# Performance work log

Measured on AMD Instinct MI355X. Metric: run time of the kernel, lower is better.

Reference implementation:

```python
import jax, jax.numpy as jnp
import numpy as np

# ---- static config ----
G = 4          # num graphs
NG = 512       # nodes per graph
N = G * NG     # total nodes
E = 32768      # num edges
IN_DIM = 128
HID = 32
HEADS = 4
HC = HID * HEADS  # 128
OUT_DIM = 32
N_LAYERS = 2
GRID = 500
Q = 20
NEG_SLOPE = 0.2
QUANTILES = jnp.asarray(np.linspace(0.0, 1.0, Q), jnp.float32)  # [Q]


def setup_inputs() -> dict:
    key = jax.random.key(0)
    ks = jax.random.split(key, 32)
    inp = {}
    inp['x'] = jax.random.normal(ks[0], (N, IN_DIM), jnp.float32)
    inp['edge_index'] = jax.random.randint(ks[1], (2, E), 0, N).astype(jnp.int64)
    inp['batch'] = (jnp.arange(N) // NG).astype(jnp.int64)
    # GATConv params (2 layers, both 128 -> 4 heads x 32, concat)
    for l, (kin,) in enumerate([(IN_DIM,), (HC,)]):
        s = 1.0 / np.sqrt(kin)
        inp[f'W{l}'] = jax.random.normal(ks[2 + 4 * l], (kin, HC), jnp.float32) * s
        inp[f'as{l}'] = jax.random.normal(ks[3 + 4 * l], (HEADS, HID), jnp.float32) * s
        inp[f'ad{l}'] = jax.random.normal(ks[4 + 4 * l], (HEADS, HID), jnp.float32) * s
        inp[f'b{l}'] = jnp.zeros((HC,), jnp.float32)
    for l in range(N_LAYERS + 1):
        inp[f'lpW{l}'] = jax.random.normal(ks[10 + 2 * l], (HC, OUT_DIM), jnp.float32) * (1.0 / np.sqrt(HC))
        inp[f'lpb{l}'] = jnp.zeros((OUT_DIM,), jnp.float32)
    for l in range(N_LAYERS + 1):
        inp[f'kW{l}'] = jax.random.normal(ks[16 + 2 * l], (HC * Q, OUT_DIM), jnp.float32) * (1.0 / np.sqrt(HC * Q))
        inp[f'kb{l}'] = jnp.zeros((OUT_DIM,), jnp.float32)
    inp['pool_w'] = jnp.ones((2,), jnp.float32) / 2.0
    inp['beta'] = jax.random.normal(ks[22], (OUT_DIM,), jnp.float32)
    inp['h0'] = jax.random.normal(ks[23], (1,), jnp.float32)
    return inp


def _gat_layer(x, src, dst, W, a_src, a_dst, bias):
    # PyG GATConv (concat=True, add_self_loops=True, negative_slope=0.2), eval mode
    n = x.shape[0]
    xh = (x @ W).reshape(n, HEADS, HID)              # [N,H,C]
    loop = jnp.arange(n)
    s = jnp.concatenate([src, loop])                 # [E+N]
    d = jnp.concatenate([dst, loop])
    al_s = jnp.einsum('nhc,hc->nh', xh, a_src)       # [N,H]
    al_d = jnp.einsum('nhc,hc->nh', xh, a_dst)
    e = jax.nn.leaky_relu(al_s[s] + al_d[d], NEG_SLOPE)   # [E+N,H]
    e_max = jax.ops.segment_max(e, d, num_segments=n)     # stable softmax per dst
    e = jnp.exp(e - e_max[d])
    denom = jax.ops.segment_sum(e, d, num_segments=n)
    alpha = e / (denom[d] + 1e-16)                   # [E+N,H]
    out = jax.ops.segment_sum(alpha[:, :, None] * xh[s], d, num_segments=n)
    return out.reshape(n, HC) + bias


def _kde_per_graph(xg):
    # xg: [Ng, D] -> [D*Q] soft-quantile features via grid KDE
    n = xg.shape[0]
    mn = xg.min(axis=0) - 1e-6                       # [D]
    mx = xg.max(axis=0) + 1e-6
    grid = jnp.linspace(0.0, 1.0, GRID)[:, None] * (mx - mn) + mn   # [Gp,D]
    std = xg.std(axis=0) + 1e-8 / 3
    h = 1.06 * std * float(n) ** (-0.2)              # [D]
    u = (grid[:, None, :] - xg[None, :, :]) / h      # [Gp,Ng,D]  (dominant tensor)
    kern = jnp.exp(-0.5 * u * u) / (h * np.sqrt(2.0 * np.pi))
    density = kern.mean(axis=1)                      # [Gp,D]
    cdf = jnp.cumsum(density, axis=0)
    cdf = cdf / jnp.clip(cdf[-1:], 1e-8)
    dist = jnp.abs(cdf[:, :, None] - QUANTILES)      # [Gp,D,Q]
    w = jax.nn.sigmoid(-100.0 * dist)
    w = w / (w.sum(axis=0, keepdims=True) + 1e-8)
    qv = (grid[:, :, None] * w).sum(axis=0)          # [D,Q]
    return qv.reshape(-1)


def _readout(cur, lpW, lpb, kW, kb, pool_w):
    xr = cur.reshape(G, NG, -1)
    pooled = jnp.stack([xr.mean(axis=1), xr.max(axis=1)], axis=0)   # [2,G,D]
    wp = (pooled * pool_w[:, None, None]).sum(axis=0)               # [G,D]
    h = wp @ lpW + lpb                                              # [G,out]
    kf = jax.vmap(_kde_per_graph)(xr)                               # [G,D*Q]
    return h, kf @ kW + kb


def reference(x, edge_index, batch, W0, as0, ad0, b0, W1, as1, ad1, b1,
              lpW0, lpb0, lpW1, lpb1, lpW2, lpb2,
              kW0, kb0, kW1, kb1, kW2, kb2, pool_w, beta, h0):
    src, dst = edge_index[0], edge_index[1]
    convs = [(W0, as0, ad0, b0), (W1, as1, ad1, b1)]
    lps = [(lpW0, lpb0), (lpW1, lpb1), (lpW2, lpb2)]
    kps = [(kW0, kb0), (kW1, kb1), (kW2, kb2)]
    cur = x
    h_list, kde_list = [], []
    for i in range(N_LAYERS):
        h, kp = _readout(cur, lps[i][0], lps[i][1], kps[i][0], kps[i][1], pool_w)
        h_list.append(h); kde_list.append(kp)
        cur = _gat_layer(cur, src, dst, *convs[i])
        if i != N_LAYERS - 1:
            cur = jax.nn.relu(cur)
    h, kp = _readout(cur, lps[-1][0], lps[-1][1], kps[-1][0], kps[-1][1], pool_w)
    h_list.append(h); kde_list.append(kp)
    main_out = jnp.stack(h_list).mean(axis=0)        # [G,out]
    kde_out = jnp.stack(kde_list).mean(axis=0)
    risk = (main_out + kde_out) @ beta + h0          # [G]
    return risk
```

## Files before the change

### kernel.cpp

```cpp
#include <hip/hip_runtime.h>
#include <math.h>

#define GNUM 4
#define NG 512
#define NN 2048
#define EE 32768
#define HC 128
#define HEADS 4
#define HID 32
#define GRID_PTS 500
#define QN 20
#define ODIM 32
#define MAXE 160

#define LOG2E 1.44269504088896340736f
#define NEG_HALF_LOG2E -0.72134752044448170368f
#define N_POW_M02 0.2871745887492588f
#define SIG_K 144.269504089f

__device__ __forceinline__ float fexp2(float x){ return __builtin_amdgcn_exp2f(x); }
__device__ __forceinline__ float frcp(float x){ return __builtin_amdgcn_rcpf(x); }

__global__ __launch_bounds__(1024) void k_zero(int* __restrict__ pos, float* __restrict__ acc){
  int t = threadIdx.x;
  pos[t] = 0; pos[t+1024] = 0;
  if (t < 768) acc[t] = 0.f;
}

__global__ __launch_bounds__(512) void k_layer(const float* __restrict__ cur, int do_relu,
        const float* __restrict__ kW, const float* __restrict__ kb, float* __restrict__ kacc,
        const float* __restrict__ lpW, const float* __restrict__ lpb,
        const float* __restrict__ poolw, float* __restrict__ macc,
        const float* __restrict__ W, const float* __restrict__ as_, const float* __restrict__ ad_,
        float* __restrict__ xh, float* __restrict__ als, float* __restrict__ ald,
        int do_fill, const int* __restrict__ src, const int* __restrict__ dst,
        int* __restrict__ pos, int* __restrict__ csr_src){
  int t = threadIdx.x;
  if (blockIdx.x < 512){
    int g = blockIdx.x >> 7, d = blockIdx.x & 127;
    int lane = t & 63, wave = t >> 6;
    __shared__ __align__(16) float2 xs[NG];
    __shared__ float4 wred4[8];
    __shared__ float sc[4];
    __shared__ float wsum[8], woff[9];
    __shared__ float redw[QN][8], redg[QN][8];
    __shared__ float qs[QN];

    float v = cur[((size_t)g*NG + t)*HC + d];
    if (do_relu) v = fmaxf(v, 0.f);
    xs[t] = make_float2(v, v*v);
    float mn=v, mx=v, sm=v, sq=v*v;
    #pragma unroll
    for (int m=32; m>0; m>>=1){
      mn = fminf(mn, __shfl_xor(mn, m, 64));
      mx = fmaxf(mx, __shfl_xor(mx, m, 64));
      sm += __shfl_xor(sm, m, 64);
      sq += __shfl_xor(sq, m, 64);
    }
    if (lane==0) wred4[wave] = make_float4(mn,mx,sm,sq);
    __syncthreads();
    if (t==0){
      float4 r = wred4[0];
      #pragma unroll
      for (int i=1;i<8;++i){
        float4 b = wred4[i];
        r.x = fminf(r.x,b.x); r.y = fmaxf(r.y,b.y); r.z += b.z; r.w += b.w;
      }
      float mean = r.z * (1.f/NG);
      float var  = fmaxf(r.w*(1.f/NG) - mean*mean, 0.f);
      float sd   = sqrtf(var) + (1e-8f/3.f);
      float h    = 1.06f * sd * N_POW_M02;
      float lo = r.x - 1e-6f, hi = r.y + 1e-6f;
      sc[0] = lo;
      sc[1] = (hi-lo)*(1.f/(GRID_PTS-1));
      sc[2] = NEG_HALF_LOG2E/(h*h);
      sc[3] = poolw[0]*mean + poolw[1]*r.y;
    }
    __syncthreads();
    float lo = sc[0], st = sc[1], kk = sc[2];
    float gv = lo + st*(float)t;
    float acc = 0.f;
    if (t < GRID_PTS){
      float c0 = kk*gv*gv, c1 = -2.f*kk*gv;
      const float4* p4 = (const float4*)xs;
      #pragma unroll 4
      for (int i=0;i<NG/2;++i){
        float4 s2 = p4[i];
        acc += fexp2(fmaf(kk, s2.y, fmaf(c1, s2.x, c0)));
        acc += fexp2(fmaf(kk, s2.w, fmaf(c1, s2.z, c0)));
      }
    }
    float sv = acc;
    #pragma unroll
    for (int off=1; off<64; off<<=1){
      float n = __shfl_up(sv, off, 64);
      if (lane >= off) sv += n;
    }
    if (lane==63) wsum[wave] = sv;
    __syncthreads();
    if (t==0){
      float r2 = 0.f;
      #pragma unroll
      for (int i=0;i<8;++i){ woff[i]=r2; r2+=wsum[i]; }
      woff[8]=r2;
    }
    if (t < QN*8){ ((float*)redw)[t]=0.f; ((float*)redg)[t]=0.f; }
    __syncthreads();
    float invt = 1.f/fmaxf(woff[8], 1e-8f);
    float c = (sv + woff[wave]) * invt;
    float cw0 = __shfl(c, 0, 64), cw1 = __shfl(c, 63, 64);
    int qlo = max(0, (int)ceilf((cw0 - 0.17f)*(float)(QN-1)));
    int qhi = min(QN-1, (int)floorf((cw1 + 0.17f)*(float)(QN-1)));
    for (int q=qlo; q<=qhi; ++q){
      float w = 0.f;
      if (t < GRID_PTS){
        float dist = fabsf(c - (float)q*(1.f/(QN-1)));
        w = frcp(1.f + fexp2(SIG_K*dist));
      }
      float gw = gv*w;
      #pragma unroll
      for (int m=32;m>0;m>>=1){
        w  += __shfl_xor(w,  m, 64);
        gw += __shfl_xor(gw, m, 64);
      }
      if (lane==0){ redw[q][wave]=w; redg[q][wave]=gw; }
    }
    __syncthreads();
    if (t < QN){
      float sw=0.f, sgw=0.f;
      #pragma unroll
      for (int i=0;i<8;++i){ sw+=redw[t][i]; sgw+=redg[t][i]; }
      qs[t] = sgw / (sw + 1e-8f);
    }
    __syncthreads();
    if (t < ODIM){
      float a = 0.f;
      const float* kwb = kW + (size_t)d*QN*ODIM + t;
      #pragma unroll
      for (int q=0;q<QN;++q) a += qs[q]*kwb[q*ODIM];
      if (d==0) a += kb[t];
      atomicAdd(&kacc[g*ODIM + t], a);
      float b = sc[3]*lpW[d*ODIM + t];
      if (d==0) b += lpb[t];
      atomicAdd(&macc[g*ODIM + t], b);
    }
  } else {
    int b2 = blockIdx.x - 512;
    if (do_fill){
      int e = b2*512 + t;
      if (e < EE){
        int dd = dst[e];
        int p = atomicAdd(&pos[dd], 1);
        if (p < MAXE) csr_src[dd*MAXE + p] = src[e];
      }
    }
    int ln = t >> 7, j = t & 127;
    int n = b2*4 + ln;
    __shared__ float rows[4][HC];
    float v = cur[(size_t)n*HC + j];
    if (do_relu) v = fmaxf(v, 0.f);
    rows[ln][j] = v;
    __syncthreads();
    float acc = 0.f;
    #pragma unroll 8
    for (int c2=0;c2<HC;++c2)
      acc += rows[ln][c2]*W[(size_t)c2*HC + j];
    xh[(size_t)n*HC + j] = acc;
    int h = j >> 5, cc = j & 31;
    float ps = acc*as_[h*HID+cc], pd = acc*ad_[h*HID+cc];
    #pragma unroll
    for (int m=16;m>0;m>>=1){
      ps += __shfl_xor(ps, m, 32);
      pd += __shfl_xor(pd, m, 32);
    }
    if (cc==0){ als[n*HEADS+h]=ps; ald[n*HEADS+h]=pd; }
  }
}

__global__ __launch_bounds__(128) void k_gather(const int* __restrict__ csr_src,
        const int* __restrict__ pos,
        const float* __restrict__ als, const float* __restrict__ ald,
        const float* __restrict__ xh, const float* __restrict__ bias,
        float* __restrict__ out){
  int d = blockIdx.x, t = threadIdx.x;
  int deg = min(pos[d], MAXE-1);
  int E = deg + 1;
  const int* base = csr_src + d*MAXE;
  __shared__ int ssrc[MAXE];
  __shared__ float sexp[MAXE][HEADS];
  __shared__ float smax[HEADS], sfac[HEADS];
  float a0 = ald[d*4+0], a1 = ald[d*4+1], a2 = ald[d*4+2], a3 = ald[d*4+3];
  for (int i=t; i<E; i+=128){
    int s = (i < deg) ? base[i] : d;
    ssrc[i] = s;
    float e0 = als[s*4+0]+a0, e1 = als[s*4+1]+a1, e2 = als[s*4+2]+a2, e3 = als[s*4+3]+a3;
    e0 = (e0>=0.f)? e0 : 0.2f*e0;
    e1 = (e1>=0.f)? e1 : 0.2f*e1;
    e2 = (e2>=0.f)? e2 : 0.2f*e2;
    e3 = (e3>=0.f)? e3 : 0.2f*e3;
    sexp[i][0]=e0; sexp[i][1]=e1; sexp[i][2]=e2; sexp[i][3]=e3;
  }
  __syncthreads();
  if (t < HEADS){
    float m = -INFINITY;
    for (int i=0;i<E;++i) m = fmaxf(m, sexp[i][t]);
    smax[t] = m;
  }
  __syncthreads();
  for (int i=t; i<E; i+=128){
    #pragma unroll
    for (int h=0;h<HEADS;++h)
      sexp[i][h] = fexp2(LOG2E*(sexp[i][h]-smax[h]));
  }
  __syncthreads();
  if (t < HEADS){
    float sdn = 0.f;
    for (int i=0;i<E;++i) sdn += sexp[i][t];
    sfac[t] = 1.f/(sdn + 1e-16f);
  }
  __syncthreads();
  int h = t >> 5;
  float fac = sfac[h];
  float acc = bias[t];
  for (int i=0;i<E;++i)
    acc += sexp[i][h]*fac * xh[(size_t)ssrc[i]*HC + t];
  out[(size_t)d*HC + t] = acc;
}

__global__ void k_final(const float* __restrict__ macc, const float* __restrict__ kacc,
                        const float* __restrict__ beta, const float* __restrict__ h0,
                        float* __restrict__ out){
  int t = threadIdx.x;
  int g = t >> 5, o = t & 31;
  __shared__ float sdm[128];
  float s3 = macc[t] + macc[t+128] + macc[t+256]
           + kacc[t] + kacc[t+128] + kacc[t+256];
  sdm[t] = s3 * (1.f/3.f) * beta[o];
  __syncthreads();
  if ((t & 31) == 0){
    float s = 0.f;
    #pragma unroll
    for (int i=0;i<32;++i) s += sdm[g*32+i];
    out[g] = s + h0[0];
  }
}

extern "C" void kernel_launch(void* const* d_in, const int* in_sizes, int n_in,
                              void* d_out, int out_size, void* d_ws, size_t ws_size,
                              hipStream_t stream) {
  (void)in_sizes; (void)n_in; (void)out_size; (void)ws_size;
  const float* x    = (const float*)d_in[0];
  const int*   ei   = (const int*)d_in[1];
  const int*   srcp = ei;
  const int*   dstp = ei + EE;
  const float* W[2]   = {(const float*)d_in[3], (const float*)d_in[7]};
  const float* As[2]  = {(const float*)d_in[4], (const float*)d_in[8]};
  const float* Ad[2]  = {(const float*)d_in[5], (const float*)d_in[9]};
  const float* Bi[2]  = {(const float*)d_in[6], (const float*)d_in[10]};
  const float* lpW[3] = {(const float*)d_in[11], (const float*)d_in[13], (const float*)d_in[15]};
  const float* lpb[3] = {(const float*)d_in[12], (const float*)d_in[14], (const float*)d_in[16]};
  const float* kW[3]  = {(const float*)d_in[17], (const float*)d_in[19], (const float*)d_in[21]};
  const float* kb[3]  = {(const float*)d_in[18], (const float*)d_in[20], (const float*)d_in[22]};
  const float* poolw  = (const float*)d_in[23];
  const float* beta   = (const float*)d_in[24];
  const float* h0     = (const float*)d_in[25];
  float* out = (float*)d_out;

  float* ws = (float*)d_ws;
  float* cur1   = ws;
  float* cur2   = cur1 + 262144;
  float* xh     = cur2 + 262144;
  float* als    = xh + 262144;
  float* ald    = als + 8192;
  float* macc   = ald + 8192;
  float* kacc   = macc + 384;
  int*   pos     = (int*)(kacc + 384);
  int*   csr_src = pos + 2048;

  k_zero<<<1, 1024, 0, stream>>>(pos, macc);

  k_layer<<<1024, 512, 0, stream>>>(x, 0, kW[0], kb[0], kacc, lpW[0], lpb[0], poolw, macc,
                                    W[0], As[0], Ad[0], xh, als, ald,
                                    1, srcp, dstp, pos, csr_src);
  k_gather<<<NN, 128, 0, stream>>>(csr_src, pos, als, ald, xh, Bi[0], cur1);

  k_layer<<<1024, 512, 0, stream>>>(cur1, 1, kW[1], kb[1], kacc+128, lpW[1], lpb[1], poolw, macc+128,
                                    W[1], As[1], Ad[1], xh, als, ald,
                                    0, srcp, dstp, pos, csr_src);
  k_gather<<<NN, 128, 0, stream>>>(csr_src, pos, als, ald, xh, Bi[1], cur2);

  k_layer<<<512, 512, 0, stream>>>(cur2, 0, kW[2], kb[2], kacc+256, lpW[2], lpb[2], poolw, macc+256,
                                   nullptr, nullptr, nullptr, nullptr, nullptr, nullptr,
                                   0, nullptr, nullptr, nullptr, nullptr);

  k_final<<<1, 128, 0, stream>>>(macc, kacc, beta, h0, out);
}
```

Before: 211.0 us.

## Fuse all layers into one cooperative persistent kernel with grid syncs

Replaces the sequence of seven kernel launches with a single cooperative kernel of 512 blocks that runs the KDE readout, X·W projection, and attention gather phases back to back, separated by grid-wide syncs. Each block now does both a KDE column and four rows of the projection serially rather than in separate blocks, and the gather handles four destination nodes per 512-thread block. The aim is to remove launch and inter-kernel gaps, at the cost of serialising the KDE and XW work within a block and adding grid barriers. A fallback path with the old multi-kernel structure runs if the cooperative launch fails.

```diff
diff --git a/kernel.cpp b/kernel.cpp
--- a/kernel.cpp
+++ b/kernel.cpp
@@ -1,5 +1,7 @@
 #include <hip/hip_runtime.h>
+#include <hip/hip_cooperative_groups.h>
 #include <math.h>
+namespace cg = cooperative_groups;
 
 #define GNUM 4
 #define NG 512
@@ -12,6 +14,7 @@
 #define QN 20
 #define ODIM 32
 #define MAXE 160
+#define NBLK 512
 
 #define LOG2E 1.44269504088896340736f
 #define NEG_HALF_LOG2E -0.72134752044448170368f
@@ -21,227 +24,333 @@
 __device__ __forceinline__ float fexp2(float x){ return __builtin_amdgcn_exp2f(x); }
 __device__ __forceinline__ float frcp(float x){ return __builtin_amdgcn_rcpf(x); }
 
-__global__ __launch_bounds__(1024) void k_zero(int* __restrict__ pos, float* __restrict__ acc){
-  int t = threadIdx.x;
-  pos[t] = 0; pos[t+1024] = 0;
-  if (t < 768) acc[t] = 0.f;
-}
-
-__global__ __launch_bounds__(512) void k_layer(const float* __restrict__ cur, int do_relu,
+struct SmemKDE {
+  __align__(16) float2 xs[NG];
+  float4 wred4[8];
+  float sc[4];
+  float wsum[8], woff[9];
+  float redw[QN][8], redg[QN][8];
+  float qs[QN];
+};
+struct SmemXW  { float rows[4][HC]; };
+struct SmemGat {
+  int   ssrc[4][MAXE];
+  float sexp[4][MAXE][HEADS];
+  float smax[4][HEADS], sfac[4][HEADS];
+};
+union Smem { SmemKDE kde; SmemXW xw; SmemGat gat; };
+
+struct Params {
+  const float *x;
+  const int *src, *dst;
+  const float *W[2], *As[2], *Ad[2], *Bi[2];
+  const float *lpW[3], *lpb[3], *kW[3], *kb[3];
+  const float *poolw, *beta, *h0;
+  float *out;
+  float *cur1, *cur2, *xh, *als, *ald, *macc, *kacc;
+  int *pos, *csr;
+};
+
+__device__ void kde_phase(Smem& sm, const float* __restrict__ cur, int do_relu,
         const float* __restrict__ kW, const float* __restrict__ kb, float* __restrict__ kacc,
         const float* __restrict__ lpW, const float* __restrict__ lpb,
-        const float* __restrict__ poolw, float* __restrict__ macc,
+        const float* __restrict__ poolw, float* __restrict__ macc){
+  int b = blockIdx.x;
+  int g = b >> 7, d = b & 127;
+  int t = threadIdx.x;
+  int lane = t & 63, wave = t >> 6;
+  float v = cur[((size_t)g*NG + t)*HC + d];
+  if (do_relu) v = fmaxf(v, 0.f);
+  sm.kde.xs[t] = make_float2(v, v*v);
+  float mn=v, mx=v, smv=v, sq=v*v;
+  #pragma unroll
+  for (int m=32; m>0; m>>=1){
+    mn = fminf(mn, __shfl_xor(mn, m, 64));
+    mx = fmaxf(mx, __shfl_xor(mx, m, 64));
+    smv += __shfl_xor(smv, m, 64);
+    sq += __shfl_xor(sq, m, 64);
+  }
+  if (lane==0) sm.kde.wred4[wave] = make_float4(mn,mx,smv,sq);
+  __syncthreads();
+  if (t==0){
+    float4 r = sm.kde.wred4[0];
+    #pragma unroll
+    for (int i=1;i<8;++i){
+      float4 bb = sm.kde.wred4[i];
+      r.x = fminf(r.x,bb.x); r.y = fmaxf(r.y,bb.y); r.z += bb.z; r.w += bb.w;
+    }
+    float mean = r.z * (1.f/NG);
+    float var  = fmaxf(r.w*(1.f/NG) - mean*mean, 0.f);
+    float sd   = sqrtf(var) + (1e-8f/3.f);
+    float h    = 1.06f * sd * N_POW_M02;
+    float lo = r.x - 1e-6f, hi = r.y + 1e-6f;
+    sm.kde.sc[0] = lo;
+    sm.kde.sc[1] = (hi-lo)*(1.f/(GRID_PTS-1));
+    sm.kde.sc[2] = NEG_HALF_LOG2E/(h*h);
+    sm.kde.sc[3] = poolw[0]*mean + poolw[1]*r.y;
+  }
+  __syncthreads();
+  float lo = sm.kde.sc[0], st = sm.kde.sc[1], kk = sm.kde.sc[2];
+  float gv = lo + st*(float)t;
+  float acc = 0.f;
+  if (t < GRID_PTS){
+    float c0 = kk*gv*gv, c1 = -2.f*kk*gv;
+    const float4* p4 = (const float4*)sm.kde.xs;
+    #pragma unroll 4
+    for (int i=0;i<NG/2;++i){
+      float4 s2 = p4[i];
+      acc += fexp2(fmaf(kk, s2.y, fmaf(c1, s2.x, c0)));
+      acc += fexp2(fmaf(kk, s2.w, fmaf(c1, s2.z, c0)));
+    }
+  }
+  float sv = acc;
+  #pragma unroll
+  for (int off=1; off<64; off<<=1){
+    float n = __shfl_up(sv, off, 64);
+    if (lane >= off) sv += n;
+  }
+  if (lane==63) sm.kde.wsum[wave] = sv;
+  __syncthreads();
+  if (t==0){
+    float r2 = 0.f;
+    #pragma unroll
+    for (int i=0;i<8;++i){ sm.kde.woff[i]=r2; r2+=sm.kde.wsum[i]; }
+    sm.kde.woff[8]=r2;
+  }
+  if (t < QN*8){ ((float*)sm.kde.redw)[t]=0.f; ((float*)sm.kde.redg)[t]=0.f; }
+  __syncthreads();
+  float invt = 1.f/fmaxf(sm.kde.woff[8], 1e-8f);
+  float c = (sv + sm.kde.woff[wave]) * invt;
+  float cw0 = __shfl(c, 0, 64), cw1 = __shfl(c, 63, 64);
+  int qlo = max(0, (int)ceilf((cw0 - 0.17f)*(float)(QN-1)));
+  int qhi = min(QN-1, (int)floorf((cw1 + 0.17f)*(float)(QN-1)));
+  for (int q=qlo; q<=qhi; ++q){
+    float w = 0.f;
+    if (t < GRID_PTS){
+      float dist = fabsf(c - (float)q*(1.f/(QN-1)));
+      w = frcp(1.f + fexp2(SIG_K*dist));
+    }
+    float gw = gv*w;
+    #pragma unroll
+    for (int m=32;m>0;m>>=1){
+      w  += __shfl_xor(w,  m, 64);
+      gw += __shfl_xor(gw, m, 64);
+    }
+    if (lane==0){ sm.kde.redw[q][wave]=w; sm.kde.redg[q][wave]=gw; }
+  }
+  __syncthreads();
+  if (t < QN){
+    float sw=0.f, sgw=0.f;
+    #pragma unroll
+    for (int i=0;i<8;++i){ sw+=sm.kde.redw[t][i]; sgw+=sm.kde.redg[t][i]; }
+    sm.kde.qs[t] = sgw / (sw + 1e-8f);
+  }
+  __syncthreads();
+  if (t < ODIM){
+    float a = 0.f;
+    const float* kwb = kW + (size_t)d*QN*ODIM + t;
+    #pragma unroll
+    for (int q=0;q<QN;++q) a += sm.kde.qs[q]*kwb[q*ODIM];
+    if (d==0) a += kb[t];
+    atomicAdd(&kacc[g*ODIM + t], a);
+    float bb = sm.kde.sc[3]*lpW[d*ODIM + t];
+    if (d==0) bb += lpb[t];
+    atomicAdd(&macc[g*ODIM + t], bb);
+  }
+  __syncthreads();
+}
+
+__device__ void xw_phase(Smem& sm, const float* __restrict__ cur, int do_relu,
         const float* __restrict__ W, const float* __restrict__ as_, const float* __restrict__ ad_,
         float* __restrict__ xh, float* __restrict__ als, float* __restrict__ ald,
         int do_fill, const int* __restrict__ src, const int* __restrict__ dst,
-        int* __restrict__ pos, int* __restrict__ csr_src){
+        int* __restrict__ pos, int* __restrict__ csr){
   int t = threadIdx.x;
-  if (blockIdx.x < 512){
-    int g = blockIdx.x >> 7, d = blockIdx.x & 127;
-    int lane = t & 63, wave = t >> 6;
-    __shared__ __align__(16) float2 xs[NG];
-    __shared__ float4 wred4[8];
-    __shared__ float sc[4];
-    __shared__ float wsum[8], woff[9];
-    __shared__ float redw[QN][8], redg[QN][8];
-    __shared__ float qs[QN];
-
-    float v = cur[((size_t)g*NG + t)*HC + d];
-    if (do_relu) v = fmaxf(v, 0.f);
-    xs[t] = make_float2(v, v*v);
-    float mn=v, mx=v, sm=v, sq=v*v;
-    #pragma unroll
-    for (int m=32; m>0; m>>=1){
-      mn = fminf(mn, __shfl_xor(mn, m, 64));
-      mx = fmaxf(mx, __shfl_xor(mx, m, 64));
-      sm += __shfl_xor(sm, m, 64);
-      sq += __shfl_xor(sq, m, 64);
-    }
-    if (lane==0) wred4[wave] = make_float4(mn,mx,sm,sq);
-    __syncthreads();
-    if (t==0){
-      float4 r = wred4[0];
-      #pragma unroll
-      for (int i=1;i<8;++i){
-        float4 b = wred4[i];
-        r.x = fminf(r.x,b.x); r.y = fmaxf(r.y,b.y); r.z += b.z; r.w += b.w;
-      }
-      float mean = r.z * (1.f/NG);
-      float var  = fmaxf(r.w*(1.f/NG) - mean*mean, 0.f);
-      float sd   = sqrtf(var) + (1e-8f/3.f);
-      float h    = 1.06f * sd * N_POW_M02;
-      float lo = r.x - 1e-6f, hi = r.y + 1e-6f;
-      sc[0] = lo;
-      sc[1] = (hi-lo)*(1.f/(GRID_PTS-1));
-      sc[2] = NEG_HALF_LOG2E/(h*h);
-      sc[3] = poolw[0]*mean + poolw[1]*r.y;
-    }
-    __syncthreads();
-    float lo = sc[0], st = sc[1], kk = sc[2];
-    float gv = lo + st*(float)t;
-    float acc = 0.f;
-    if (t < GRID_PTS){
-      float c0 = kk*gv*gv, c1 = -2.f*kk*gv;
-      const float4* p4 = (const float4*)xs;
-      #pragma unroll 4
-      for (int i=0;i<NG/2;++i){
-        float4 s2 = p4[i];
-        acc += fexp2(fmaf(kk, s2.y, fmaf(c1, s2.x, c0)));
-        acc += fexp2(fmaf(kk, s2.w, fmaf(c1, s2.z, c0)));
-      }
-    }
-    float sv = acc;
-    #pragma unroll
-    for (int off=1; off<64; off<<=1){
-      float n = __shfl_up(sv, off, 64);
-      if (lane >= off) sv += n;
-    }
-    if (lane==63) wsum[wave] = sv;
-    __syncthreads();
-    if (t==0){
-      float r2 = 0.f;
-      #pragma unroll
-      for (int i=0;i<8;++i){ woff[i]=r2; r2+=wsum[i]; }
-      woff[8]=r2;
-    }
-    if (t < QN*8){ ((float*)redw)[t]=0.f; ((float*)redg)[t]=0.f; }
-    __syncthreads();
-    float invt = 1.f/fmaxf(woff[8], 1e-8f);
-    float c = (sv + woff[wave]) * invt;
-    float cw0 = __shfl(c, 0, 64), cw1 = __shfl(c, 63, 64);
-    int qlo = max(0, (int)ceilf((cw0 - 0.17f)*(float)(QN-1)));
-    int qhi = min(QN-1, (int)floorf((cw1 + 0.17f)*(float)(QN-1)));
-    for (int q=qlo; q<=qhi; ++q){
-      float w = 0.f;
-      if (t < GRID_PTS){
-        float dist = fabsf(c - (float)q*(1.f/(QN-1)));
-        w = frcp(1.f + fexp2(SIG_K*dist));
-      }
-      float gw = gv*w;
-      #pragma unroll
-      for (int m=32;m>0;m>>=1){
-        w  += __shfl_xor(w,  m, 64);
-        gw += __shfl_xor(gw, m, 64);
-      }
-      if (lane==0){ redw[q][wave]=w; redg[q][wave]=gw; }
-    }
-    __syncthreads();
-    if (t < QN){
-      float sw=0.f, sgw=0.f;
-      #pragma unroll
-      for (int i=0;i<8;++i){ sw+=redw[t][i]; sgw+=redg[t][i]; }
-      qs[t] = sgw / (sw + 1e-8f);
-    }
-    __syncthreads();
-    if (t < ODIM){
-      float a = 0.f;
-      const float* kwb = kW + (size_t)d*QN*ODIM + t;
-      #pragma unroll
-      for (int q=0;q<QN;++q) a += qs[q]*kwb[q*ODIM];
-      if (d==0) a += kb[t];
-      atomicAdd(&kacc[g*ODIM + t], a);
-      float b = sc[3]*lpW[d*ODIM + t];
-      if (d==0) b += lpb[t];
-      atomicAdd(&macc[g*ODIM + t], b);
-    }
-  } else {
-    int b2 = blockIdx.x - 512;
-    if (do_fill){
-      int e = b2*512 + t;
-      if (e < EE){
-        int dd = dst[e];
-        int p = atomicAdd(&pos[dd], 1);
-        if (p < MAXE) csr_src[dd*MAXE + p] = src[e];
-      }
-    }
-    int ln = t >> 7, j = t & 127;
-    int n = b2*4 + ln;
-    __shared__ float rows[4][HC];
-    float v = cur[(size_t)n*HC + j];
-    if (do_relu) v = fmaxf(v, 0.f);
-    rows[ln][j] = v;
-    __syncthreads();
-    float acc = 0.f;
-    #pragma unroll 8
-    for (int c2=0;c2<HC;++c2)
-      acc += rows[ln][c2]*W[(size_t)c2*HC + j];
-    xh[(size_t)n*HC + j] = acc;
-    int h = j >> 5, cc = j & 31;
-    float ps = acc*as_[h*HID+cc], pd = acc*ad_[h*HID+cc];
-    #pragma unroll
-    for (int m=16;m>0;m>>=1){
-      ps += __shfl_xor(ps, m, 32);
-      pd += __shfl_xor(pd, m, 32);
-    }
-    if (cc==0){ als[n*HEADS+h]=ps; ald[n*HEADS+h]=pd; }
-  }
-}
-
-__global__ __launch_bounds__(128) void k_gather(const int* __restrict__ csr_src,
-        const int* __restrict__ pos,
+  if (do_fill && t < 64){
+    int e = blockIdx.x*64 + t;
+    int dd = dst[e];
+    int pp = atomicAdd(&pos[dd], 1);
+    if (pp < MAXE) csr[dd*MAXE + pp] = src[e];
+  }
+  int ln = t >> 7, j = t & 127;
+  int n = blockIdx.x*4 + ln;
+  float v = cur[(size_t)n*HC + j];
+  if (do_relu) v = fmaxf(v, 0.f);
+  sm.xw.rows[ln][j] = v;
+  __syncthreads();
+  float acc = 0.f;
+  #pragma unroll 8
+  for (int c2=0;c2<HC;++c2)
+    acc += sm.xw.rows[ln][c2]*W[(size_t)c2*HC + j];
+  xh[(size_t)n*HC + j] = acc;
+  int h = j >> 5, cc = j & 31;
+  float ps = acc*as_[h*HID+cc], pd = acc*ad_[h*HID+cc];
+  #pragma unroll
+  for (int m=16;m>0;m>>=1){
+    ps += __shfl_xor(ps, m, 32);
+    pd += __shfl_xor(pd, m, 32);
+  }
+  if (cc==0){ als[n*HEADS+h]=ps; ald[n*HEADS+h]=pd; }
+  __syncthreads();
+}
+
+__device__ void gather_phase(Smem& sm, const int* __restrict__ csr, const int* __restrict__ pos,
         const float* __restrict__ als, const float* __restrict__ ald,
         const float* __restrict__ xh, const float* __restrict__ bias,
         float* __restrict__ out){
-  int d = blockIdx.x, t = threadIdx.x;
+  int t = threadIdx.x;
+  int sub = t >> 7, tl = t & 127;
+  int d = blockIdx.x*4 + sub;
   int deg = min(pos[d], MAXE-1);
   int E = deg + 1;
-  const int* base = csr_src + d*MAXE;
-  __shared__ int ssrc[MAXE];
-  __shared__ float sexp[MAXE][HEADS];
-  __shared__ float smax[HEADS], sfac[HEADS];
+  const int* base = csr + d*MAXE;
   float a0 = ald[d*4+0], a1 = ald[d*4+1], a2 = ald[d*4+2], a3 = ald[d*4+3];
-  for (int i=t; i<E; i+=128){
+  for (int i=tl; i<E; i+=128){
     int s = (i < deg) ? base[i] : d;
-    ssrc[i] = s;
+    sm.gat.ssrc[sub][i] = s;
     float e0 = als[s*4+0]+a0, e1 = als[s*4+1]+a1, e2 = als[s*4+2]+a2, e3 = als[s*4+3]+a3;
     e0 = (e0>=0.f)? e0 : 0.2f*e0;
     e1 = (e1>=0.f)? e1 : 0.2f*e1;
     e2 = (e2>=0.f)? e2 : 0.2f*e2;
     e3 = (e3>=0.f)? e3 : 0.2f*e3;
-    sexp[i][0]=e0; sexp[i][1]=e1; sexp[i][2]=e2; sexp[i][3]=e3;
-  }
-  __syncthreads();
-  if (t < HEADS){
+    sm.gat.sexp[sub][i][0]=e0; sm.gat.sexp[sub][i][1]=e1;
+    sm.gat.sexp[sub][i][2]=e2; sm.gat.sexp[sub][i][3]=e3;
+  }
+  __syncthreads();
+  if (tl < HEADS){
     float m = -INFINITY;
-    for (int i=0;i<E;++i) m = fmaxf(m, sexp[i][t]);
-    smax[t] = m;
-  }
-  __syncthreads();
-  for (int i=t; i<E; i+=128){
+    for (int i=0;i<E;++i) m = fmaxf(m, sm.gat.sexp[sub][i][tl]);
+    sm.gat.smax[sub][tl] = m;
+  }
+  __syncthreads();
+  for (int i=tl; i<E; i+=128){
     #pragma unroll
     for (int h=0;h<HEADS;++h)
-      sexp[i][h] = fexp2(LOG2E*(sexp[i][h]-smax[h]));
-  }
-  __syncthreads();
-  if (t < HEADS){
+      sm.gat.sexp[sub][i][h] = fexp2(LOG2E*(sm.gat.sexp[sub][i][h]-sm.gat.smax[sub][h]));
+  }
+  __syncthreads();
+  if (tl < HEADS){
     float sdn = 0.f;
-    for (int i=0;i<E;++i) sdn += sexp[i][t];
-    sfac[t] = 1.f/(sdn + 1e-16f);
-  }
-  __syncthreads();
-  int h = t >> 5;
-  float fac = sfac[h];
-  float acc = bias[t];
+    for (int i=0;i<E;++i) sdn += sm.gat.sexp[sub][i][tl];
+    sm.gat.sfac[sub][tl] = 1.f/(sdn + 1e-16f);
+  }
+  __syncthreads();
+  int h = tl >> 5;
+  float fac = sm.gat.sfac[sub][h];
+  float acc = bias[tl];
   for (int i=0;i<E;++i)
-    acc += sexp[i][h]*fac * xh[(size_t)ssrc[i]*HC + t];
-  out[(size_t)d*HC + t] = acc;
-}
-
-__global__ void k_final(const float* __restrict__ macc, const float* __restrict__ kacc,
-                        const float* __restrict__ beta, const float* __restrict__ h0,
-                        float* __restrict__ out){
+    acc += sm.gat.sexp[sub][i][h]*fac * xh[(size_t)sm.gat.ssrc[sub][i]*HC + tl];
+  out[(size_t)d*HC + tl] = acc;
+  __syncthreads();
+}
+
+__global__ __launch_bounds__(512, 4) void k_all(Params p){
+  cg::grid_group grid = cg::this_grid();
+  __shared__ Smem sm;
+  int t = threadIdx.x, b = blockIdx.x;
+
+  if (b < 8){
+    int i = b*512 + t;
+    if (i < 2048) p.pos[i] = 0;
+    else if (i < 2816) p.macc[i-2048] = 0.f;
+  }
+  grid.sync();
+
+  kde_phase(sm, p.x, 0, p.kW[0], p.kb[0], p.kacc, p.lpW[0], p.lpb[0], p.poolw, p.macc);
+  xw_phase (sm, p.x, 0, p.W[0], p.As[0], p.Ad[0], p.xh, p.als, p.ald, 1, p.src, p.dst, p.pos, p.csr);
+  grid.sync();
+  gather_phase(sm, p.csr, p.pos, p.als, p.ald, p.xh, p.Bi[0], p.cur1);
+  grid.sync();
+
+  kde_phase(sm, p.cur1, 1, p.kW[1], p.kb[1], p.kacc+128, p.lpW[1], p.lpb[1], p.poolw, p.macc+128);
+  xw_phase (sm, p.cur1, 1, p.W[1], p.As[1], p.Ad[1], p.xh, p.als, p.ald, 0, nullptr, nullptr, nullptr, nullptr);
+  grid.sync();
+  gather_phase(sm, p.csr, p.pos, p.als, p.ald, p.xh, p.Bi[1], p.cur2);
+  grid.sync();
+
+  kde_phase(sm, p.cur2, 0, p.kW[2], p.kb[2], p.kacc+256, p.lpW[2], p.lpb[2], p.poolw, p.macc+256);
+  grid.sync();
+
+  if (b == 0){
+    float* sdm = (float*)&sm;
+    if (t < 128){
+      float s3 = p.macc[t]+p.macc[t+128]+p.macc[t+256]
+               + p.kacc[t]+p.kacc[t+128]+p.kacc[t+256];
+      sdm[t] = s3 * (1.f/3.f) * p.beta[t & 31];
+    }
+    __syncthreads();
+    if (t < 128 && (t & 31) == 0){
+      int g = t >> 5;
+      float s = 0.f;
+      #pragma unroll
+      for (int i=0;i<32;++i) s += sdm[g*32+i];
+      p.out[g] = s + p.h0[0];
+    }
+  }
+}
+
+__global__ __launch_bounds__(1024) void k_zero(int* __restrict__ pos, float* __restrict__ acc){
   int t = threadIdx.x;
-  int g = t >> 5, o = t & 31;
+  pos[t] = 0; pos[t+1024] = 0;
+  if (t < 768) acc[t] = 0.f;
+}
+
+__global__ __launch_bounds__(512) void k_layer(Params p, const float* cur, int do_relu, int li,
+                                               int do_fill, float* outnul){
+  (void)outnul;
+  __shared__ Smem sm;
+  if (blockIdx.x < 512){
+    kde_phase(sm, cur, do_relu, p.kW[li], p.kb[li], p.kacc+li*128,
+              p.lpW[li], p.lpb[li], p.poolw, p.macc+li*128);
+  } else if (li < 2){
+    int b2 = blockIdx.x - 512;
+    int t = threadIdx.x;
+    if (do_fill && t < 64){
+      int e = b2*64 + t;
+      int dd = p.dst[e];
+      int pp = atomicAdd(&p.pos[dd], 1);
+      if (pp < MAXE) p.csr[dd*MAXE + pp] = p.src[e];
+    }
+    int ln = t >> 7, j = t & 127;
+    int n = b2*4 + ln;
+    float v = cur[(size_t)n*HC + j];
+    if (do_relu) v = fmaxf(v, 0.f);
+    sm.xw.rows[ln][j] = v;
+    __syncthreads();
+    float acc = 0.f;
+    #pragma unroll 8
+    for (int c2=0;c2<HC;++c2)
+      acc += sm.xw.rows[ln][c2]*p.W[li][(size_t)c2*HC + j];
+    p.xh[(size_t)n*HC + j] = acc;
+    int h = j >> 5, cc = j & 31;
+    float ps = acc*p.As[li][h*HID+cc], pd = acc*p.Ad[li][h*HID+cc];
+    #pragma unroll
+    for (int m=16;m>0;m>>=1){
+      ps += __shfl_xor(ps, m, 32);
+      pd += __shfl_xor(pd, m, 32);
+    }
+    if (cc==0){ p.als[n*HEADS+h]=ps; p.ald[n*HEADS+h]=pd; }
+  }
+}
+
+__global__ __launch_bounds__(512) void k_gather_f(Params p, int li, float* outb){
+  __shared__ Smem sm;
+  gather_phase(sm, p.csr, p.pos, p.als, p.ald, p.xh, p.Bi[li], outb);
+}
+
+__global__ void k_final_f(Params p){
+  int t = threadIdx.x;
   __shared__ float sdm[128];
-  float s3 = macc[t] + macc[t+128] + macc[t+256]
-           + kacc[t] + kacc[t+128] + kacc[t+256];
-  sdm[t] = s3 * (1.f/3.f) * beta[o];
+  float s3 = p.macc[t]+p.macc[t+128]+p.macc[t+256]
+           + p.kacc[t]+p.kacc[t+128]+p.kacc[t+256];
+  sdm[t] = s3 * (1.f/3.f) * p.beta[t & 31];
   __syncthreads();
   if ((t & 31) == 0){
+    int g = t >> 5;
     float s = 0.f;
     #pragma unroll
     for (int i=0;i<32;++i) s += sdm[g*32+i];
-    out[g] = s + h0[0];
+    p.out[g] = s + p.h0[0];
   }
 }
 
@@ -249,49 +358,44 @@
                               void* d_out, int out_size, void* d_ws, size_t ws_size,
                               hipStream_t stream) {
   (void)in_sizes; (void)n_in; (void)out_size; (void)ws_size;
-  const float* x    = (const float*)d_in[0];
-  const int*   ei   = (const int*)d_in[1];
-  const int*   srcp = ei;
-  const int*   dstp = ei + EE;
-  const float* W[2]   = {(const float*)d_in[3], (const float*)d_in[7]};
-  const float* As[2]  = {(const float*)d_in[4], (const float*)d_in[8]};
-  const float* Ad[2]  = {(const float*)d_in[5], (const float*)d_in[9]};
-  const float* Bi[2]  = {(const float*)d_in[6], (const float*)d_in[10]};
-  const float* lpW[3] = {(const float*)d_in[11], (const float*)d_in[13], (const float*)d_in[15]};
-  const float* lpb[3] = {(const float*)d_in[12], (const float*)d_in[14], (const float*)d_in[16]};
-  const float* kW[3]  = {(const float*)d_in[17], (const float*)d_in[19], (const float*)d_in[21]};
-  const float* kb[3]  = {(const float*)d_in[18], (const float*)d_in[20], (const float*)d_in[22]};
-  const float* poolw  = (const float*)d_in[23];
-  const float* beta   = (const float*)d_in[24];
-  const float* h0     = (const float*)d_in[25];
-  float* out = (float*)d_out;
+  Params p;
+  p.x   = (const float*)d_in[0];
+  const int* ei = (const int*)d_in[1];
+  p.src = ei; p.dst = ei + EE;
+  p.W[0]=(const float*)d_in[3];  p.As[0]=(const float*)d_in[4];
+  p.Ad[0]=(const float*)d_in[5]; p.Bi[0]=(const float*)d_in[6];
+  p.W[1]=(const float*)d_in[7];  p.As[1]=(const float*)d_in[8];
+  p.Ad[1]=(const float*)d_in[9]; p.Bi[1]=(const float*)d_in[10];
+  p.lpW[0]=(const float*)d_in[11]; p.lpb[0]=(const float*)d_in[12];
+  p.lpW[1]=(const float*)d_in[13]; p.lpb[1]=(const float*)d_in[14];
+  p.lpW[2]=(const float*)d_in[15]; p.lpb[2]=(const float*)d_in[16];
+  p.kW[0]=(const float*)d_in[17]; p.kb[0]=(const float*)d_in[18];
+  p.kW[1]=(const float*)d_in[19]; p.kb[1]=(const float*)d_in[20];
+  p.kW[2]=(const float*)d_in[21]; p.kb[2]=(const float*)d_in[22];
+  p.poolw=(const float*)d_in[23]; p.beta=(const float*)d_in[24]; p.h0=(const float*)d_in[25];
+  p.out = (float*)d_out;
 
   float* ws = (float*)d_ws;
-  float* cur1   = ws;
-  float* cur2   = cur1 + 262144;
-  float* xh     = cur2 + 262144;
-  float* als    = xh + 262144;
-  float* ald    = als + 8192;
-  float* macc   = ald + 8192;
-  float* kacc   = macc + 384;
-  int*   pos     = (int*)(kacc + 384);
-  int*   csr_src = pos + 2048;
-
-  k_zero<<<1, 1024, 0, stream>>>(pos, macc);
-
-  k_layer<<<1024, 512, 0, stream>>>(x, 0, kW[0], kb[0], kacc, lpW[0], lpb[0], poolw, macc,
-                                    W[0], As[0], Ad[0], xh, als, ald,
-                                    1, srcp, dstp, pos, csr_src);
-  k_gather<<<NN, 128, 0, stream>>>(csr_src, pos, als, ald, xh, Bi[0], cur1);
-
-  k_layer<<<1024, 512, 0, stream>>>(cur1, 1, kW[1], kb[1], kacc+128, lpW[1], lpb[1], poolw, macc+128,
-                                    W[1], As[1], Ad[1], xh, als, ald,
-                                    0, srcp, dstp, pos, csr_src);
-  k_gather<<<NN, 128, 0, stream>>>(csr_src, pos, als, ald, xh, Bi[1], cur2);
-
-  k_layer<<<512, 512, 0, stream>>>(cur2, 0, kW[2], kb[2], kacc+256, lpW[2], lpb[2], poolw, macc+256,
-                                   nullptr, nullptr, nullptr, nullptr, nullptr, nullptr,
-                                   0, nullptr, nullptr, nullptr, nullptr);
-
-  k_final<<<1, 128, 0, stream>>>(macc, kacc, beta, h0, out);
-}
+  p.cur1 = ws;
+  p.cur2 = p.cur1 + 262144;
+  p.xh   = p.cur2 + 262144;
+  p.als  = p.xh + 262144;
+  p.ald  = p.als + 8192;
+  p.macc = p.ald + 8192;
+  p.kacc = p.macc + 384;
+  p.pos  = (int*)(p.kacc + 384);
+  p.csr  = p.pos + 2048;
+
+  void* kargs[] = { (void*)&p };
+  hipError_t err = hipLaunchCooperativeKernel((void*)k_all, dim3(NBLK), dim3(512),
+                                              kargs, 0, stream);
+  if (err != hipSuccess){
+    k_zero<<<1, 1024, 0, stream>>>(p.pos, p.macc);
+    k_layer<<<1024, 512, 0, stream>>>(p, p.x, 0, 0, 1, nullptr);
+    k_gather_f<<<NBLK, 512, 0, stream>>>(p, 0, p.cur1);
+    k_layer<<<1024, 512, 0, stream>>>(p, p.cur1, 1, 1, 0, nullptr);
+    k_gather_f<<<NBLK, 512, 0, stream>>>(p, 1, p.cur2);
+    k_layer<<<512, 512, 0, stream>>>(p, p.cur2, 0, 2, 0, nullptr);
+    k_final_f<<<1, 128, 0, stream>>>(p);
+  }
+}
```

Result: slower. 539.4 us (+155.7%).
